# Kernel optimization log

Measured on AMD Instinct MI355X. Metric: run time of the kernel, lower is better.

## Reference

```python
import jax, jax.numpy as jnp
import numpy as np

B, S, D, H, F, REF = 4, 1024, 512, 8, 2048, 2
HGRID = 32   # sqrt(seq_len)
HALF = 3     # 7x7 window -> half-width 3


def _masks():
    i = jnp.arange(HGRID)
    near = jnp.abs(i[:, None] - i[None, :]) <= HALF            # [h,h]
    inside = (near[:, None, :, None] & near[None, :, None, :]).reshape(S, S)
    # reverse=True mask (mca): outside-window -> -inf, inside -> 0
    m_rev = jnp.where(inside, 0.0, -jnp.inf).astype(jnp.float32)
    # reverse=False mask (msa/nsa): inside-window -> -inf, outside -> 0 (faithful to source)
    m_fwd = jnp.where(inside, -jnp.inf, 0.0).astype(jnp.float32)
    return m_rev, m_fwd


def _mha(q, k, v, w, b, ow, ob, mask):
    # torch nn.MultiheadAttention, batch_first, eval mode (no dropout)
    hd = D // H
    wq, wk, wv = jnp.split(w, 3, axis=0)
    bq, bk, bv = jnp.split(b, 3)

    def proj(t, wt, bt):
        Bt, Lt = t.shape[0], t.shape[1]
        return (t @ wt.T + bt).reshape(Bt, Lt, H, hd).transpose(0, 2, 1, 3)

    qh, kh, vh = proj(q, wq, bq), proj(k, wk, bk), proj(v, wv, bv)
    scores = jnp.einsum('bhqd,bhkd->bhqk', qh, kh) / jnp.sqrt(jnp.float32(hd))
    if mask is not None:
        scores = scores + mask
    a = jax.nn.softmax(scores, axis=-1)
    o = jnp.einsum('bhqk,bhkd->bhqd', a, vh).transpose(0, 2, 1, 3).reshape(q.shape[0], q.shape[1], D)
    return o @ ow.T + ob


def _ln(x, g, b, eps=1e-5):
    m = x.mean(-1, keepdims=True)
    v = ((x - m) ** 2).mean(-1, keepdims=True)
    return (x - m) / jnp.sqrt(v + eps) * g + b


def setup_inputs() -> dict:
    key = jax.random.key(0)
    ks = jax.random.split(key, 16)
    d = {}
    d['x'] = jax.random.normal(ks[0], (B, S, D), jnp.float32)
    d['ref_mca'] = jax.random.normal(ks[1], (B, REF * S, D), jnp.float32)
    d['gate'] = jax.random.uniform(ks[2], (B, S, 5), jnp.float32)
    i = 3
    for p in ['mca', 'ca', 'msa', 'nsa', 'sa']:
        d[p + '_w'] = 0.02 * jax.random.normal(ks[i], (3 * D, D), jnp.float32); i += 1
        d[p + '_b'] = jnp.zeros((3 * D,), jnp.float32)
        d[p + '_ow'] = 0.02 * jax.random.normal(ks[i], (D, D), jnp.float32); i += 1
        d[p + '_ob'] = jnp.zeros((D,), jnp.float32)
    d['ln1_g'] = jnp.ones((D,), jnp.float32); d['ln1_b'] = jnp.zeros((D,), jnp.float32)
    d['ln2_g'] = jnp.ones((D,), jnp.float32); d['ln2_b'] = jnp.zeros((D,), jnp.float32)
    d['fc1_w'] = 0.02 * jax.random.normal(ks[i], (F, D), jnp.float32); i += 1
    d['fc1_b'] = jnp.zeros((F,), jnp.float32)
    d['fc2_w'] = 0.02 * jax.random.normal(ks[i], (D, F), jnp.float32); i += 1
    d['fc2_b'] = jnp.zeros((D,), jnp.float32)
    return d


def reference(x, ref_mca, gate,
              mca_w, mca_b, mca_ow, mca_ob,
              ca_w, ca_b, ca_ow, ca_ob,
              msa_w, msa_b, msa_ow, msa_ob,
              nsa_w, nsa_b, nsa_ow, nsa_ob,
              sa_w, sa_b, sa_ow, sa_ob,
              ln1_g, ln1_b, ln2_g, ln2_b,
              fc1_w, fc1_b, fc2_w, fc2_b):
    m_rev, m_fwd = _masks()
    # mca branch: sum attention over each seq_len chunk of ref_mca (window-inside mask)
    mca_x = jnp.zeros_like(x)
    for r in range(REF):
        chunk = ref_mca[:, r * S:(r + 1) * S, :]
        mca_x = mca_x + _mha(x, chunk, chunk, mca_w, mca_b, mca_ow, mca_ob, m_rev)
    # faithful to source: loop variable leaks, so ca/nsa use the LAST chunk
    ref_last = ref_mca[:, (REF - 1) * S:, :]
    new_x = gate[:, :, 0:1] * mca_x
    new_x = new_x + gate[:, :, 1:2] * _mha(x, ref_last, ref_last, ca_w, ca_b, ca_ow, ca_ob, None)
    new_x = new_x + gate[:, :, 2:3] * _mha(x, x, x, msa_w, msa_b, msa_ow, msa_ob, m_fwd)
    new_x = new_x + gate[:, :, 3:4] * _mha(x, ref_last, x, nsa_w, nsa_b, nsa_ow, nsa_ob, m_fwd)
    new_x = new_x + gate[:, :, 4:5] * _mha(x, x, x, sa_w, sa_b, sa_ow, sa_ob, None)
    h = _ln(new_x, ln1_g, ln1_b)
    y = jax.nn.gelu(h @ fc1_w.T + fc1_b, approximate=False) @ fc2_w.T + fc2_b
    return _ln(h + y, ln2_g, ln2_b)
```

## Files before the change

kernel.cpp:

```cpp
#include <hip/hip_runtime.h>

typedef __bf16 bf16_t;
typedef bf16_t bf16x8 __attribute__((ext_vector_type(8)));
typedef float f32x4v __attribute__((ext_vector_type(4)));
typedef unsigned int u32;
typedef unsigned long long u64;

__device__ __forceinline__ void gload16(const bf16_t* g, bf16_t* l) {
    __builtin_amdgcn_global_load_lds((const __attribute__((address_space(1))) u32*)g,
                                     (__attribute__((address_space(3))) u32*)l, 16, 0, 0);
}

#define QSCALE 0.18033688011112042f

struct PackBDesc {
    int nseg;
    int blkOf[21];
    const float* src[20];
    bf16_t* dst[20];
    int chunks[20];
    int dstLd[20];
    int shift[20];
};

__global__ __launch_bounds__(256) void packb_k(PackBDesc d) {
    int b = blockIdx.x;
    int s = 0;
    while (s + 1 < d.nseg && b >= d.blkOf[s + 1]) ++s;
    int idx = (b - d.blkOf[s]) * 256 + threadIdx.x;
    if (idx >= d.chunks[s]) return;
    const float* src = d.src[s] + (size_t)idx * 8;
    int r = idx >> d.shift[s];
    int c8 = idx & ((1 << d.shift[s]) - 1);
    bf16_t* dst = d.dst[s] + (size_t)r * d.dstLd[s] + (size_t)c8 * 8;
    float4 v0 = reinterpret_cast<const float4*>(src)[0];
    float4 v1 = reinterpret_cast<const float4*>(src)[1];
    bf16x8 o;
    o[0] = (bf16_t)v0.x; o[1] = (bf16_t)v0.y; o[2] = (bf16_t)v0.z; o[3] = (bf16_t)v0.w;
    o[4] = (bf16_t)v1.x; o[5] = (bf16_t)v1.y; o[6] = (bf16_t)v1.z; o[7] = (bf16_t)v1.w;
    *reinterpret_cast<bf16x8*>(dst) = o;
}

struct PackFDesc {
    int nseg;
    int blkOf[15];
    const float* src[14];
    float* dst[14];
    int n[14];
};

__global__ __launch_bounds__(256) void packf_k(PackFDesc d) {
    int b = blockIdx.x;
    int s = 0;
    while (s + 1 < d.nseg && b >= d.blkOf[s + 1]) ++s;
    int idx = (b - d.blkOf[s]) * 256 + threadIdx.x;
    if (idx >= d.n[s]) return;
    d.dst[s][idx] = d.src[s][idx];
}

template <int EPI, int BM, int BN>
__device__ __forceinline__ void gemm_core(
    int tm, int tn, int bz,
    const bf16_t* __restrict__ A, int aBS, int aRowOff, int lda,
    const bf16_t* __restrict__ B,
    const float* __restrict__ bias,
    void* __restrict__ Out, int ldo, size_t outSplitStride,
    const float* __restrict__ gate, const float* __restrict__ obcat,
    int kStart, int kLen, u64 scaleMask) {
    constexpr int MB = BM / 32, NB = BN / 32, WM = BM / 2, WN = BN / 2;
    constexpr int CA = BM / 64, CB = BN / 64;
    __shared__ __attribute__((aligned(16))) bf16_t As[2][BM * 32];
    __shared__ __attribute__((aligned(16))) bf16_t Bs[2][BN * 32];
    const int tid = threadIdx.x, lane = tid & 63, w = tid >> 6;
    const int wm = w >> 1, wn = w & 1;
    const int l15 = lane & 15, l16 = lane >> 4;
    const int colS = (lane & 3) * 8, rowS = lane >> 2;

    auto remap = [&](int m) { return (m >> 10) * aBS + aRowOff + (m & 1023); };

    const bf16_t* aS[CA];
    const bf16_t* bS[CB];
#pragma unroll
    for (int c = 0; c < CA; ++c)
        aS[c] = A + (size_t)remap(tm * BM + (CA * w + c) * 16 + rowS) * lda + kStart + colS;
#pragma unroll
    for (int c = 0; c < CB; ++c)
        bS[c] = B + (size_t)(tn * BN + (CB * w + c) * 16 + rowS) * lda + kStart + colS;

    auto stage = [&](int buf, int t) {
        const size_t o = (size_t)t * 32;
#pragma unroll
        for (int c = 0; c < CA; ++c) gload16(aS[c] + o, &As[buf][(CA * w + c) * 512]);
#pragma unroll
        for (int c = 0; c < CB; ++c) gload16(bS[c] + o, &Bs[buf][(CB * w + c) * 512]);
    };

    f32x4v acc[MB][NB] = {};
    const int nt = kLen / 32;
    stage(0, 0);
    __syncthreads();
    int cur = 0;
    for (int t = 0; t < nt; ++t) {
        if (t + 1 < nt) stage(cur ^ 1, t + 1);
        bf16x8 af[MB], bff[NB];
#pragma unroll
        for (int mi = 0; mi < MB; ++mi)
            af[mi] = *reinterpret_cast<const bf16x8*>(&As[cur][(wm * WM + mi * 16 + l15) * 32 + l16 * 8]);
#pragma unroll
        for (int ni = 0; ni < NB; ++ni)
            bff[ni] = *reinterpret_cast<const bf16x8*>(&Bs[cur][(wn * WN + ni * 16 + l15) * 32 + l16 * 8]);
#pragma unroll
        for (int mi = 0; mi < MB; ++mi)
#pragma unroll
            for (int ni = 0; ni < NB; ++ni)
                acc[mi][ni] = __builtin_amdgcn_mfma_f32_16x16x32_bf16(af[mi], bff[ni], acc[mi][ni], 0, 0, 0);
        __syncthreads();
        cur ^= 1;
    }

    const bool doScale = (EPI == 0) && ((scaleMask >> tn) & 1ULL);
#pragma unroll
    for (int mi = 0; mi < MB; ++mi) {
#pragma unroll
        for (int ni = 0; ni < NB; ++ni) {
#pragma unroll
            for (int i = 0; i < 4; ++i) {
                int row = tm * BM + wm * WM + mi * 16 + l16 * 4 + i;
                int n = tn * BN + wn * WN + ni * 16 + l15;
                float v = acc[mi][ni][i];
                if (bias && bz == 0) v += bias[n];
                if constexpr (EPI == 0) {
                    if (doScale) v *= QSCALE;
                    ((bf16_t*)Out)[(size_t)row * ldo + n] = (bf16_t)v;
                } else if constexpr (EPI == 1) {
                    float g = 0.5f * v * (1.0f + erff(v * 0.70710678118654752f));
                    ((bf16_t*)Out)[(size_t)row * ldo + n] = (bf16_t)g;
                } else if constexpr (EPI == 3) {
                    ((float*)Out + (size_t)bz * outSplitStride)[(size_t)row * ldo + n] = v;
                } else {
                    if (obcat && bz == 0) {
#pragma unroll
                        for (int p = 0; p < 5; ++p) {
                            float c = (p == 0) ? 2.0f : 1.0f;
                            v += gate[row * 5 + p] * c * obcat[p * 512 + n];
                        }
                    }
                    ((float*)Out + (size_t)bz * outSplitStride)[(size_t)row * ldo + n] = v;
                }
            }
        }
    }
}

struct ProjDesc {
    const bf16_t* A[3];
    int aBS[3], aRowOff[3];
    const bf16_t* B[3];
    const float* bias[3];
    bf16_t* Out[3];
    int ldo[3];
    int ntn[3], base[3];
    u64 qmask[3];
};

__global__ __launch_bounds__(256) void proj_k(ProjDesc d) {
    int wg = (blockIdx.x & 7) * 272 + (blockIdx.x >> 3);
    int s = (wg >= d.base[2]) ? 2 : (wg >= d.base[1]) ? 1 : 0;
    int local = wg - d.base[s];
    int tn = local % d.ntn[s];
    int tm = local / d.ntn[s];
    gemm_core<0, 128, 128>(tm, tn, 0, d.A[s], d.aBS[s], d.aRowOff[s], 512,
                           d.B[s], d.bias[s], d.Out[s], d.ldo[s], 0, nullptr, nullptr, 0, 512,
                           d.qmask[s]);
}

template <int EPI, int BM, int BN>
__global__ __launch_bounds__(256) void gemmT(
    const bf16_t* __restrict__ A, int aBS, int aRowOff, int lda,
    const bf16_t* __restrict__ B, const float* __restrict__ bias,
    void* __restrict__ Out, int ldo, size_t outSplitStride,
    const float* __restrict__ gate, const float* __restrict__ obcat, int kPerSplit) {
    gemm_core<EPI, BM, BN>(blockIdx.y, blockIdx.x, blockIdx.z, A, aBS, aRowOff, lda, B, bias,
                           Out, ldo, outSplitStride, gate, obcat, blockIdx.z * kPerSplit, kPerSplit, 0);
}

struct AttnDesc {
    const bf16_t* Q[6];
    const bf16_t* K[6];
    const bf16_t* V[6];
    int ldq[6], ldk[6], ldv[6];
    int segOff[6], gidx[6], mask[6];
    bf16_t* acat;
    const float* gate;
};

__global__ __launch_bounds__(512, 4) void attn6_k(AttnDesc d) {
    __shared__ __attribute__((aligned(16))) bf16_t Ks[64][72];
    __shared__ __attribute__((aligned(16))) bf16_t Vt[64][72];
    __shared__ __attribute__((aligned(16))) bf16_t Ps[8][2][16][40];

    const int bid = blockIdx.x;
    const int xcd = bid & 7;
    const int qt = (bid >> 3) & 3;
    const int gg = bid >> 5;
    const int g = gg * 8 + xcd;
    const int u = g >> 5, lg = g & 31;
    const int mask = d.mask[u];
    const int h = lg & 7, b = lg >> 3;

    const int tid = threadIdx.x;
    const int lane = tid & 63;
    const int w = tid >> 6;
    const int l15 = lane & 15, l16 = lane >> 4;

    const int qbase = qt * 256 + w * 32;
    const int qrow = b * 1024 + qbase;
    const int qblk = qbase >> 5;
    const int ldq = d.ldq[u], ldk = d.ldk[u], ldv = d.ldv[u];

    bf16x8 aq[2][2];
#pragma unroll
    for (int t = 0; t < 2; ++t)
#pragma unroll
        for (int s = 0; s < 2; ++s)
            aq[t][s] = *reinterpret_cast<const bf16x8*>(
                d.Q[u] + (size_t)(qrow + t * 16 + l15) * ldq + h * 64 + s * 32 + l16 * 8);

    float mrow0 = -1e30f, mrow1 = -1e30f, lsum0 = 0.f, lsum1 = 0.f;
    f32x4v accO[2][4] = {};

    const int srow = tid >> 3, scol8 = (tid & 7) * 8;
    const int vcol = srow ^ ((tid & 7) << 3);
    const bf16_t* kbase = d.K[u] + (size_t)(b * 1024) * ldk + h * 64 + scol8;
    const bf16_t* vbase = d.V[u] + (size_t)(b * 1024) * ldv + h * 64 + scol8;

    int t0, t1;
    if (mask == 1) {
        int klo = qt * 8 - 3;  if (klo < 0) klo = 0;
        int khi = qt * 8 + 10; if (khi > 31) khi = 31;
        t0 = klo >> 1; t1 = (khi >> 1) + 1;
    } else { t0 = 0; t1 = 16; }

    bf16x8 rk, rv, rk2, rv2;
    rk = *reinterpret_cast<const bf16x8*>(kbase + (size_t)(t0 * 64 + srow) * ldk);
    rv = *reinterpret_cast<const bf16x8*>(vbase + (size_t)(t0 * 64 + srow) * ldv);

    for (int tt = t0; tt < t1; ++tt) {
        __syncthreads();
        *reinterpret_cast<bf16x8*>(&Ks[srow][scol8]) = rk;
#pragma unroll
        for (int j = 0; j < 8; ++j) Vt[scol8 + j][vcol] = rv[j];
        if (tt + 1 < t1) {
            rk2 = *reinterpret_cast<const bf16x8*>(kbase + (size_t)((tt + 1) * 64 + srow) * ldk);
            rv2 = *reinterpret_cast<const bf16x8*>(vbase + (size_t)((tt + 1) * 64 + srow) * ldv);
        }
        __syncthreads();

        int bd0 = qblk - tt * 2;     if (bd0 < 0) bd0 = -bd0;
        int bd1 = qblk - tt * 2 - 1; if (bd1 < 0) bd1 = -bd1;
        const bool a0 = (mask != 1) || (bd0 <= 3);
        const bool a1 = (mask != 1) || (bd1 <= 3);
        if (a0 || a1) {
            f32x4v z[2][4];
#pragma unroll
            for (int nt = 0; nt < 4; ++nt) {
                bf16x8 kf0 = *reinterpret_cast<const bf16x8*>(&Ks[nt * 16 + l15][l16 * 8]);
                bf16x8 kf1 = *reinterpret_cast<const bf16x8*>(&Ks[nt * 16 + l15][32 + l16 * 8]);
                f32x4v z0 = {}, z1 = {};
                z0 = __builtin_amdgcn_mfma_f32_16x16x32_bf16(kf0, aq[0][0], z0, 0, 0, 0);
                z0 = __builtin_amdgcn_mfma_f32_16x16x32_bf16(kf1, aq[0][1], z0, 0, 0, 0);
                z1 = __builtin_amdgcn_mfma_f32_16x16x32_bf16(kf0, aq[1][0], z1, 0, 0, 0);
                z1 = __builtin_amdgcn_mfma_f32_16x16x32_bf16(kf1, aq[1][1], z1, 0, 0, 0);
                z[0][nt] = z0; z[1][nt] = z1;
            }
            float p[2][4][4];
#pragma unroll
            for (int t = 0; t < 2; ++t) {
                const int qgt = t * 16 + l15;
#pragma unroll
                for (int nt = 0; nt < 4; ++nt) {
                    const int bd = (nt >> 1) ? bd1 : bd0;
                    const bool act = (nt >> 1) ? a1 : a0;
                    const bool needMask = (mask == 1) || (mask == 2 && bd <= 3);
#pragma unroll
                    for (int i = 0; i < 4; ++i) {
                        float v = z[t][nt][i];
                        if (!act) v = -1e30f;
                        else if (needMask) {
                            int k5 = (nt & 1) * 16 + l16 * 4 + i;
                            int dq = qgt - k5; if (dq < 0) dq = -dq;
                            bool inside = (bd <= 3) && (dq <= 3);
                            if (mask == 1 ? !inside : inside) v = -1e30f;
                        }
                        p[t][nt][i] = v;
                    }
                }
            }
            float tmx0 = p[0][0][0], tmx1 = p[1][0][0];
#pragma unroll
            for (int nt = 0; nt < 4; ++nt)
#pragma unroll
                for (int i = 0; i < 4; ++i) {
                    tmx0 = fmaxf(tmx0, p[0][nt][i]);
                    tmx1 = fmaxf(tmx1, p[1][nt][i]);
                }
            tmx0 = fmaxf(tmx0, __shfl_xor(tmx0, 16, 64));
            tmx0 = fmaxf(tmx0, __shfl_xor(tmx0, 32, 64));
            tmx1 = fmaxf(tmx1, __shfl_xor(tmx1, 16, 64));
            tmx1 = fmaxf(tmx1, __shfl_xor(tmx1, 32, 64));
            float grow = fmaxf(tmx0 - mrow0, tmx1 - mrow1);
            if (!__all(grow <= 8.0f)) {
                float mn0 = fmaxf(mrow0, tmx0), mn1 = fmaxf(mrow1, tmx1);
                float f0 = exp2f(mrow0 - mn0), f1 = exp2f(mrow1 - mn1);
                mrow0 = mn0; mrow1 = mn1;
                lsum0 *= f0; lsum1 *= f1;
                float fq0[4], fq1[4];
#pragma unroll
                for (int i = 0; i < 4; ++i) {
                    fq0[i] = __shfl(f0, l16 * 4 + i, 64);
                    fq1[i] = __shfl(f1, l16 * 4 + i, 64);
                }
#pragma unroll
                for (int dblk = 0; dblk < 4; ++dblk)
#pragma unroll
                    for (int i = 0; i < 4; ++i) {
                        accO[0][dblk][i] *= fq0[i];
                        accO[1][dblk][i] *= fq1[i];
                    }
            }
            float rs0 = 0.f, rs1 = 0.f;
#pragma unroll
            for (int nt = 0; nt < 4; ++nt)
#pragma unroll
                for (int i = 0; i < 4; ++i) {
                    p[0][nt][i] = exp2f(p[0][nt][i] - mrow0); rs0 += p[0][nt][i];
                    p[1][nt][i] = exp2f(p[1][nt][i] - mrow1); rs1 += p[1][nt][i];
                }
            rs0 += __shfl_xor(rs0, 16, 64); rs0 += __shfl_xor(rs0, 32, 64);
            rs1 += __shfl_xor(rs1, 16, 64); rs1 += __shfl_xor(rs1, 32, 64);
            lsum0 += rs0; lsum1 += rs1;

#pragma unroll
            for (int kh = 0; kh < 2; ++kh) {
#pragma unroll
                for (int n = 0; n < 2; ++n)
#pragma unroll
                    for (int i = 0; i < 4; ++i) {
                        Ps[w][0][l15][n * 16 + l16 * 4 + i] = (bf16_t)p[0][kh * 2 + n][i];
                        Ps[w][1][l15][n * 16 + l16 * 4 + i] = (bf16_t)p[1][kh * 2 + n][i];
                    }
                bf16x8 pa0 = *reinterpret_cast<const bf16x8*>(&Ps[w][0][l15][l16 * 8]);
                bf16x8 pa1 = *reinterpret_cast<const bf16x8*>(&Ps[w][1][l15][l16 * 8]);
#pragma unroll
                for (int dblk = 0; dblk < 4; ++dblk) {
                    int dd = dblk * 16 + l15;
                    int csw = ((kh * 4 + l16) ^ (dd >> 3)) * 8;
                    bf16x8 bv = *reinterpret_cast<const bf16x8*>(&Vt[dd][csw]);
                    accO[0][dblk] = __builtin_amdgcn_mfma_f32_16x16x32_bf16(pa0, bv, accO[0][dblk], 0, 0, 0);
                    accO[1][dblk] = __builtin_amdgcn_mfma_f32_16x16x32_bf16(pa1, bv, accO[1][dblk], 0, 0, 0);
                }
            }
        }
        rk = rk2; rv = rv2;
    }

    float inv0 = 1.0f / lsum0, inv1 = 1.0f / lsum1;
    float iq0[4], iq1[4];
#pragma unroll
    for (int i = 0; i < 4; ++i) {
        iq0[i] = __shfl(inv0, l16 * 4 + i, 64);
        iq1[i] = __shfl(inv1, l16 * 4 + i, 64);
    }
#pragma unroll
    for (int dblk = 0; dblk < 4; ++dblk)
#pragma unroll
        for (int i = 0; i < 4; ++i) {
            int r0 = qrow + l16 * 4 + i;
            int r1 = r0 + 16;
            float g0 = d.gate[(size_t)r0 * 5 + d.gidx[u]];
            float g1 = d.gate[(size_t)r1 * 5 + d.gidx[u]];
            d.acat[(size_t)r0 * 3072 + d.segOff[u] + h * 64 + dblk * 16 + l15] =
                (bf16_t)(accO[0][dblk][i] * iq0[i] * g0);
            d.acat[(size_t)r1 * 3072 + d.segOff[u] + h * 64 + dblk * 16 + l15] =
                (bf16_t)(accO[1][dblk][i] * iq1[i] * g1);
        }
}

__global__ __launch_bounds__(256) void ln_k(const float* __restrict__ in0,
                                            const float* __restrict__ in1,
                                            const float* __restrict__ in2,
                                            const float* __restrict__ g,
                                            const float* __restrict__ bb,
                                            float* __restrict__ outf,
                                            bf16_t* __restrict__ outb) {
    __shared__ float red[8];
    int row = blockIdx.x;
    int t = threadIdx.x;
    float x0 = in0[(size_t)row * 512 + t];
    float x1 = in0[(size_t)row * 512 + 256 + t];
    if (in1) {
        x0 += in1[(size_t)row * 512 + t];
        x1 += in1[(size_t)row * 512 + 256 + t];
    }
    if (in2) {
        x0 += in2[(size_t)row * 512 + t];
        x1 += in2[(size_t)row * 512 + 256 + t];
    }
    float s = x0 + x1, sq = x0 * x0 + x1 * x1;
#pragma unroll
    for (int d = 1; d < 64; d <<= 1) {
        s += __shfl_xor(s, d, 64);
        sq += __shfl_xor(sq, d, 64);
    }
    int w = t >> 6;
    if ((t & 63) == 0) { red[w] = s; red[4 + w] = sq; }
    __syncthreads();
    s = red[0] + red[1] + red[2] + red[3];
    sq = red[4] + red[5] + red[6] + red[7];
    float mean = s * (1.0f / 512.0f);
    float var = sq * (1.0f / 512.0f) - mean * mean;
    float rstd = rsqrtf(var + 1e-5f);
    float y0 = (x0 - mean) * rstd * g[t] + bb[t];
    float y1 = (x1 - mean) * rstd * g[256 + t] + bb[256 + t];
    if (outf) {
        outf[(size_t)row * 512 + t] = y0;
        outf[(size_t)row * 512 + 256 + t] = y1;
    }
    if (outb) {
        outb[(size_t)row * 512 + t] = (bf16_t)y0;
        outb[(size_t)row * 512 + 256 + t] = (bf16_t)y1;
    }
}

extern "C" void kernel_launch(void* const* d_in, const int* in_sizes, int n_in,
                              void* d_out, int out_size, void* d_ws, size_t ws_size,
                              hipStream_t stream) {
    (void)in_sizes; (void)n_in; (void)out_size; (void)ws_size;
    const float* x       = (const float*)d_in[0];
    const float* ref_mca = (const float*)d_in[1];
    const float* gate    = (const float*)d_in[2];
    const float *w[5], *wb[5], *ow[5], *ob[5];
    for (int p = 0; p < 5; ++p) {
        w[p]  = (const float*)d_in[3 + p * 4];
        wb[p] = (const float*)d_in[4 + p * 4];
        ow[p] = (const float*)d_in[5 + p * 4];
        ob[p] = (const float*)d_in[6 + p * 4];
    }
    const float* ln1_g = (const float*)d_in[23];
    const float* ln1_b = (const float*)d_in[24];
    const float* ln2_g = (const float*)d_in[25];
    const float* ln2_b = (const float*)d_in[26];
    const float* fc1_w = (const float*)d_in[27];
    const float* fc1_b = (const float*)d_in[28];
    const float* fc2_w = (const float*)d_in[29];
    const float* fc2_b = (const float*)d_in[30];

    char* ws = (char*)d_ws;
    size_t off = 0;
    auto alloc = [&](size_t bytes) {
        char* p = ws + off;
        off += (bytes + 255) & ~(size_t)255;
        return p;
    };
    const size_t S2 = (size_t)4096 * 512;
    bf16_t* xb    = (bf16_t*)alloc(S2 * 2);
    bf16_t* refb  = (bf16_t*)alloc((size_t)8192 * 512 * 2);
    bf16_t* Wxp   = (bf16_t*)alloc((size_t)5120 * 512 * 2);
    bf16_t* WRp   = (bf16_t*)alloc((size_t)2560 * 512 * 2);
    bf16_t* Wop   = (bf16_t*)alloc((size_t)512 * 3072 * 2);
    bf16_t* fc1p  = (bf16_t*)alloc((size_t)2048 * 512 * 2);
    bf16_t* fc2p  = (bf16_t*)alloc((size_t)512 * 2048 * 2);
    float*  bxp   = (float*)alloc((size_t)5120 * 4);
    float*  brp   = (float*)alloc((size_t)2560 * 4);
    float*  obc   = (float*)alloc((size_t)5 * 512 * 4);
    bf16_t* XP    = (bf16_t*)alloc((size_t)4096 * 5120 * 2);
    bf16_t* RP    = (bf16_t*)alloc((size_t)4096 * 2560 * 2);
    bf16_t* R0    = (bf16_t*)alloc((size_t)4096 * 1024 * 2);
    bf16_t* acat  = (bf16_t*)alloc((size_t)4096 * 3072 * 2);
    float*  newx  = (float*)alloc(S2 * 4 * 2);
    float*  hbuf  = (float*)alloc(S2 * 4);
    bf16_t* hb  = refb;
    bf16_t* ub  = XP;
    float*  yp  = newx;

    PackBDesc pb{};
    int nb = 0, blk = 0;
    auto addB = [&](const float* s, bf16_t* dptr, int chunks, int dstLd, int shift) {
        pb.src[nb] = s; pb.dst[nb] = dptr; pb.chunks[nb] = chunks;
        pb.dstLd[nb] = dstLd; pb.shift[nb] = shift;
        pb.blkOf[nb] = blk; blk += (chunks + 255) / 256; ++nb;
    };
    auto addLin = [&](const float* s, bf16_t* dptr, long elems) {
        addB(s, dptr, (int)(elems / 8), 0, 30);
    };
    addLin(x, xb, (long)4096 * 512);
    addLin(ref_mca, refb, (long)8192 * 512);
    addLin(w[0], Wxp, (long)512 * 512);
    addLin(w[1], Wxp + (size_t)512 * 512, (long)512 * 512);
    addLin(w[2], Wxp + (size_t)1024 * 512, (long)1536 * 512);
    addLin(w[3], Wxp + (size_t)2560 * 512, (long)512 * 512);
    addLin(w[3] + (size_t)1024 * 512, Wxp + (size_t)3072 * 512, (long)512 * 512);
    addLin(w[4], Wxp + (size_t)3584 * 512, (long)1536 * 512);
    addLin(w[0] + (size_t)512 * 512, WRp, (long)1024 * 512);
    addLin(w[1] + (size_t)512 * 512, WRp + (size_t)1024 * 512, (long)1024 * 512);
    addLin(w[3] + (size_t)512 * 512, WRp + (size_t)2048 * 512, (long)512 * 512);
    const float* owSeg[6] = {ow[0], ow[0], ow[1], ow[2], ow[3], ow[4]};
    for (int s = 0; s < 6; ++s)
        addB(owSeg[s], Wop + (size_t)s * 512, 32768, 3072, 6);
    addLin(fc1_w, fc1p, (long)2048 * 512);
    addLin(fc2_w, fc2p, (long)512 * 2048);
    pb.nseg = nb; pb.blkOf[nb] = blk;
    packb_k<<<blk, 256, 0, stream>>>(pb);

    PackFDesc pf{};
    int nf = 0, fblk = 0;
    auto addF = [&](const float* s, float* dptr, int n) {
        pf.src[nf] = s; pf.dst[nf] = dptr; pf.n[nf] = n;
        pf.blkOf[nf] = fblk; fblk += (n + 255) / 256; ++nf;
    };
    addF(wb[0], bxp, 512);
    addF(wb[1], bxp + 512, 512);
    addF(wb[2], bxp + 1024, 1536);
    addF(wb[3], bxp + 2560, 512);
    addF(wb[3] + 1024, bxp + 3072, 512);
    addF(wb[4], bxp + 3584, 1536);
    addF(wb[0] + 512, brp, 1024);
    addF(wb[1] + 512, brp + 1024, 1024);
    addF(wb[3] + 512, brp + 2048, 512);
    for (int p = 0; p < 5; ++p) addF(ob[p], obc + p * 512, 512);
    pf.nseg = nf; pf.blkOf[nf] = fblk;
    packf_k<<<fblk, 256, 0, stream>>>(pf);

    ProjDesc pd{};
    pd.A[0] = xb;   pd.aBS[0] = 1024; pd.aRowOff[0] = 0;    pd.B[0] = Wxp; pd.bias[0] = bxp; pd.Out[0] = XP; pd.ldo[0] = 5120; pd.ntn[0] = 40;
    pd.A[1] = refb; pd.aBS[1] = 2048; pd.aRowOff[1] = 1024; pd.B[1] = WRp; pd.bias[1] = brp; pd.Out[1] = RP; pd.ldo[1] = 2560; pd.ntn[1] = 20;
    pd.A[2] = refb; pd.aBS[2] = 2048; pd.aRowOff[2] = 0;    pd.B[2] = WRp; pd.bias[2] = brp; pd.Out[2] = R0; pd.ldo[2] = 1024; pd.ntn[2] = 8;
    pd.base[0] = 0; pd.base[1] = 40 * 32; pd.base[2] = 40 * 32 + 20 * 32;
    pd.qmask[0] = 0xF0F00FFFULL; pd.qmask[1] = 0; pd.qmask[2] = 0;
    proj_k<<<(40 + 20 + 8) * 32, 256, 0, stream>>>(pd);

    AttnDesc ad{};
    auto setU = [&](int u, const bf16_t* Q, int lq, const bf16_t* K, int lk,
                    const bf16_t* V, int lv, int seg, int gi, int mk) {
        ad.Q[u] = Q; ad.ldq[u] = lq; ad.K[u] = K; ad.ldk[u] = lk; ad.V[u] = V; ad.ldv[u] = lv;
        ad.segOff[u] = seg; ad.gidx[u] = gi; ad.mask[u] = mk;
    };
    setU(0, XP, 5120, R0, 1024, R0 + 512, 1024, 0, 0, 1);
    setU(1, XP, 5120, RP, 2560, RP + 512, 2560, 512, 0, 1);
    setU(2, XP + 512, 5120, RP + 1024, 2560, RP + 1536, 2560, 1024, 1, 0);
    setU(3, XP + 1024, 5120, XP + 1536, 5120, XP + 2048, 5120, 1536, 2, 2);
    setU(4, XP + 2560, 5120, RP + 2048, 2560, XP + 3072, 5120, 2048, 3, 2);
    setU(5, XP + 3584, 5120, XP + 4096, 5120, XP + 4608, 5120, 2560, 4, 0);
    ad.acat = acat; ad.gate = gate;
    attn6_k<<<768, 512, 0, stream>>>(ad);

    gemmT<4, 64, 64><<<dim3(8, 64, 2), 256, 0, stream>>>(acat, 1024, 0, 3072, Wop, nullptr,
                                                         newx, 512, S2, gate, obc, 1536);
    ln_k<<<4096, 256, 0, stream>>>(newx, newx + S2, nullptr, ln1_g, ln1_b, hbuf, hb);
    gemmT<1, 128, 128><<<dim3(16, 32, 1), 256, 0, stream>>>(hb, 1024, 0, 512, fc1p, fc1_b,
                                                            ub, 2048, 0, nullptr, nullptr, 512);
    gemmT<3, 64, 64><<<dim3(8, 64, 2), 256, 0, stream>>>(ub, 1024, 0, 2048, fc2p, fc2_b,
                                                         yp, 512, S2, nullptr, nullptr, 1024);
    ln_k<<<4096, 256, 0, stream>>>(hbuf, yp, yp + S2, ln2_g, ln2_b, (float*)d_out, nullptr);
}
```

Before: 313.1 us.

## Double-buffer K/V tiles in attention kernel and interleave unit block mapping

Result: slower. 351.2 us (+12.2%).

```diff
diff --git a/kernel.cpp b/kernel.cpp
--- a/kernel.cpp
+++ b/kernel.cpp
@@ -194,19 +194,18 @@
     const float* gate;
 };
 
-__global__ __launch_bounds__(512, 4) void attn6_k(AttnDesc d) {
-    __shared__ __attribute__((aligned(16))) bf16_t Ks[64][72];
-    __shared__ __attribute__((aligned(16))) bf16_t Vt[64][72];
-    __shared__ __attribute__((aligned(16))) bf16_t Ps[8][2][16][40];
+__global__ __launch_bounds__(512) void attn7_k(AttnDesc d) {
+    __shared__ __attribute__((aligned(16))) bf16_t Ks[2][64][72];
+    __shared__ __attribute__((aligned(16))) bf16_t Vt[2][64][72];
+    __shared__ __attribute__((aligned(16))) bf16_t Ps[8][16][40];
 
     const int bid = blockIdx.x;
-    const int xcd = bid & 7;
-    const int qt = (bid >> 3) & 3;
-    const int gg = bid >> 5;
-    const int g = gg * 8 + xcd;
-    const int u = g >> 5, lg = g & 31;
+    const int u = bid % 6;
+    const int rem = bid / 6;
+    const int qt = rem & 3;
+    const int lg = rem >> 2;
+    const int h = lg & 7, b = lg >> 3;
     const int mask = d.mask[u];
-    const int h = lg & 7, b = lg >> 3;
 
     const int tid = threadIdx.x;
     const int lane = tid & 63;
@@ -241,20 +240,24 @@
         t0 = klo >> 1; t1 = (khi >> 1) + 1;
     } else { t0 = 0; t1 = 16; }
 
+    auto ldKV = [&](int tt, bf16x8& k, bf16x8& v) {
+        k = *reinterpret_cast<const bf16x8*>(kbase + (size_t)(tt * 64 + srow) * ldk);
+        v = *reinterpret_cast<const bf16x8*>(vbase + (size_t)(tt * 64 + srow) * ldv);
+    };
+    auto stKV = [&](int buf, const bf16x8& k, const bf16x8& v) {
+        *reinterpret_cast<bf16x8*>(&Ks[buf][srow][scol8]) = k;
+#pragma unroll
+        for (int j = 0; j < 8; ++j) Vt[buf][scol8 + j][vcol] = v[j];
+    };
+
     bf16x8 rk, rv, rk2, rv2;
-    rk = *reinterpret_cast<const bf16x8*>(kbase + (size_t)(t0 * 64 + srow) * ldk);
-    rv = *reinterpret_cast<const bf16x8*>(vbase + (size_t)(t0 * 64 + srow) * ldv);
-
+    ldKV(t0, rk, rv);
+    stKV(0, rk, rv);
+    __syncthreads();
+
+    int cur = 0;
     for (int tt = t0; tt < t1; ++tt) {
-        __syncthreads();
-        *reinterpret_cast<bf16x8*>(&Ks[srow][scol8]) = rk;
-#pragma unroll
-        for (int j = 0; j < 8; ++j) Vt[scol8 + j][vcol] = rv[j];
-        if (tt + 1 < t1) {
-            rk2 = *reinterpret_cast<const bf16x8*>(kbase + (size_t)((tt + 1) * 64 + srow) * ldk);
-            rv2 = *reinterpret_cast<const bf16x8*>(vbase + (size_t)((tt + 1) * 64 + srow) * ldv);
-        }
-        __syncthreads();
+        if (tt + 1 < t1) ldKV(tt + 1, rk2, rv2);
 
         int bd0 = qblk - tt * 2;     if (bd0 < 0) bd0 = -bd0;
         int bd1 = qblk - tt * 2 - 1; if (bd1 < 0) bd1 = -bd1;
@@ -264,8 +267,8 @@
             f32x4v z[2][4];
 #pragma unroll
             for (int nt = 0; nt < 4; ++nt) {
-                bf16x8 kf0 = *reinterpret_cast<const bf16x8*>(&Ks[nt * 16 + l15][l16 * 8]);
-                bf16x8 kf1 = *reinterpret_cast<const bf16x8*>(&Ks[nt * 16 + l15][32 + l16 * 8]);
+                bf16x8 kf0 = *reinterpret_cast<const bf16x8*>(&Ks[cur][nt * 16 + l15][l16 * 8]);
+                bf16x8 kf1 = *reinterpret_cast<const bf16x8*>(&Ks[cur][nt * 16 + l15][32 + l16 * 8]);
                 f32x4v z0 = {}, z1 = {};
                 z0 = __builtin_amdgcn_mfma_f32_16x16x32_bf16(kf0, aq[0][0], z0, 0, 0, 0);
                 z0 = __builtin_amdgcn_mfma_f32_16x16x32_bf16(kf1, aq[0][1], z0, 0, 0, 0);
@@ -345,23 +348,29 @@
 #pragma unroll
                 for (int n = 0; n < 2; ++n)
 #pragma unroll
-                    for (int i = 0; i < 4; ++i) {
-                        Ps[w][0][l15][n * 16 + l16 * 4 + i] = (bf16_t)p[0][kh * 2 + n][i];
-                        Ps[w][1][l15][n * 16 + l16 * 4 + i] = (bf16_t)p[1][kh * 2 + n][i];
-                    }
-                bf16x8 pa0 = *reinterpret_cast<const bf16x8*>(&Ps[w][0][l15][l16 * 8]);
-                bf16x8 pa1 = *reinterpret_cast<const bf16x8*>(&Ps[w][1][l15][l16 * 8]);
+                    for (int i = 0; i < 4; ++i)
+                        Ps[w][l15][n * 16 + l16 * 4 + i] = (bf16_t)p[0][kh * 2 + n][i];
+                bf16x8 pa0 = *reinterpret_cast<const bf16x8*>(&Ps[w][l15][l16 * 8]);
+#pragma unroll
+                for (int n = 0; n < 2; ++n)
+#pragma unroll
+                    for (int i = 0; i < 4; ++i)
+                        Ps[w][l15][n * 16 + l16 * 4 + i] = (bf16_t)p[1][kh * 2 + n][i];
+                bf16x8 pa1 = *reinterpret_cast<const bf16x8*>(&Ps[w][l15][l16 * 8]);
 #pragma unroll
                 for (int dblk = 0; dblk < 4; ++dblk) {
                     int dd = dblk * 16 + l15;
                     int csw = ((kh * 4 + l16) ^ (dd >> 3)) * 8;
-                    bf16x8 bv = *reinterpret_cast<const bf16x8*>(&Vt[dd][csw]);
+                    bf16x8 bv = *reinterpret_cast<const bf16x8*>(&Vt[cur][dd][csw]);
                     accO[0][dblk] = __builtin_amdgcn_mfma_f32_16x16x32_bf16(pa0, bv, accO[0][dblk], 0, 0, 0);
                     accO[1][dblk] = __builtin_amdgcn_mfma_f32_16x16x32_bf16(pa1, bv, accO[1][dblk], 0, 0, 0);
                 }
             }
         }
-        rk = rk2; rv = rv2;
+
+        if (tt + 1 < t1) stKV(cur ^ 1, rk2, rv2);
+        __syncthreads();
+        cur ^= 1;
     }
 
     float inv0 = 1.0f / lsum0, inv1 = 1.0f / lsum1;
@@ -552,7 +561,7 @@
     setU(4, XP + 2560, 5120, RP + 2048, 2560, XP + 3072, 5120, 2048, 3, 2);
     setU(5, XP + 3584, 5120, XP + 4096, 5120, XP + 4608, 5120, 2560, 4, 0);
     ad.acat = acat; ad.gate = gate;
-    attn6_k<<<768, 512, 0, stream>>>(ad);
+    attn7_k<<<768, 512, 0, stream>>>(ad);
 
     gemmT<4, 64, 64><<<dim3(8, 64, 2), 256, 0, stream>>>(acat, 1024, 0, 3072, Wop, nullptr,
                                                          newx, 512, S2, gate, obc, 1536);
```
